# Kernel optimization log

Hardware: AMD Instinct MI355X
Metric: run time of the kernel (lower is better)

Reference implementation:

```python
import jax, jax.numpy as jnp
import numpy as np

N = 10000
E = 160000
IN_CH = 128
HID = 128
HEADS = 4
OUT_CH = 1  # forced by nn.Linear(heads, 1) applied after conv2


def _linear_params(key, out_f, in_f):
    k1, k2 = jax.random.split(key)
    bound = 1.0 / np.sqrt(in_f)
    W = jax.random.uniform(k1, (out_f, in_f), jnp.float32, -bound, bound)
    b = jax.random.uniform(k2, (out_f,), jnp.float32, -bound, bound)
    return W, b


def setup_inputs() -> dict:
    key = jax.random.key(0)
    ks = jax.random.split(key, 12)
    x = jax.random.normal(ks[0], (N, IN_CH), jnp.float32)
    edge_index = jax.random.randint(ks[1], (2, E), 0, N, jnp.int64)

    # conv1: TransformerConv(IN_CH, HID, HEADS)
    Wq1, bq1 = _linear_params(ks[2], HEADS * HID, IN_CH)
    Wk1, bk1 = _linear_params(ks[3], HEADS * HID, IN_CH)
    Wv1, bv1 = _linear_params(ks[4], HEADS * HID, IN_CH)
    Ws1, bs1 = _linear_params(ks[5], HEADS * HID, IN_CH)  # root/skip

    # conv2: TransformerConv(HID*HEADS, OUT_CH, HEADS)
    d2 = HID * HEADS
    Wq2, bq2 = _linear_params(ks[6], HEADS * OUT_CH, d2)
    Wk2, bk2 = _linear_params(ks[7], HEADS * OUT_CH, d2)
    Wv2, bv2 = _linear_params(ks[8], HEADS * OUT_CH, d2)
    Ws2, bs2 = _linear_params(ks[9], HEADS * OUT_CH, d2)

    # final nn.Linear(HEADS, 1)
    Wl, bl = _linear_params(ks[10], 1, HEADS)

    return dict(x=x, edge_index=edge_index,
                Wq1=Wq1, bq1=bq1, Wk1=Wk1, bk1=bk1, Wv1=Wv1, bv1=bv1, Ws1=Ws1, bs1=bs1,
                Wq2=Wq2, bq2=bq2, Wk2=Wk2, bk2=bk2, Wv2=Wv2, bv2=bv2, Ws2=Ws2, bs2=bs2,
                Wl=Wl, bl=bl)


def transformer_conv(x, edge_index, Wq, bq, Wk, bk, Wv, bv, Ws, bs, heads, ch):
    # PyG TransformerConv defaults: concat=True, root_weight=True, beta=False
    n = x.shape[0]
    q = (x @ Wq.T + bq).reshape(n, heads, ch)
    k = (x @ Wk.T + bk).reshape(n, heads, ch)
    v = (x @ Wv.T + bv).reshape(n, heads, ch)

    src, dst = edge_index[0], edge_index[1]  # messages flow src -> dst
    # per-edge attention logits [E, H]
    logits = jnp.einsum('ehc,ehc->eh', q[dst], k[src]) / np.sqrt(ch).astype(np.float32)

    # segment softmax over edges grouped by destination node
    seg_max = jax.ops.segment_max(logits, dst, num_segments=n)  # [N, H]
    seg_max = jnp.where(jnp.isfinite(seg_max), seg_max, 0.0)
    ex = jnp.exp(logits - seg_max[dst])
    denom = jax.ops.segment_sum(ex, dst, num_segments=n)  # [N, H]
    alpha = ex / jnp.maximum(denom[dst], 1e-16)  # [E, H]

    # scatter-aggregate weighted values
    msgs = alpha[:, :, None] * v[src]  # [E, H, C]
    out = jax.ops.segment_sum(msgs, dst, num_segments=n)  # [N, H, C]
    out = out.reshape(n, heads * ch)
    # root/skip connection
    return out + (x @ Ws.T + bs)


def reference(x, edge_index,
              Wq1, bq1, Wk1, bk1, Wv1, bv1, Ws1, bs1,
              Wq2, bq2, Wk2, bk2, Wv2, bv2, Ws2, bs2,
              Wl, bl):
    h = transformer_conv(x, edge_index, Wq1, bq1, Wk1, bk1, Wv1, bv1, Ws1, bs1, HEADS, HID)
    h = jax.nn.relu(h)
    # dropout is identity in eval mode
    h = transformer_conv(h, edge_index, Wq2, bq2, Wk2, bk2, Wv2, bv2, Ws2, bs2, HEADS, OUT_CH)
    h = h @ Wl.T + bl  # [N, 1]
    return jnp.mean(h, axis=0, keepdims=True)  # [1, 1]
```

## Files before the change

### kernel.cpp

```cpp
#include <hip/hip_runtime.h>
#include <math.h>

#define NN 10000
#define NE 160000
#define NROWT 79
#define NCOLT 16
#define NGEMM (NROWT * NCOLT)

typedef __attribute__((ext_vector_type(8))) short bf16x8;
typedef __attribute__((ext_vector_type(4))) float f32x4;
typedef __attribute__((ext_vector_type(2))) float f32x2;

#if defined(__has_builtin)
#if __has_builtin(__builtin_amdgcn_cvt_pk_fp8_f32) && __has_builtin(__builtin_amdgcn_cvt_pk_f32_fp8)
#define HW_FP8 1
#endif
#endif

__device__ inline ushort f2bf(float x) {
  uint u = __float_as_uint(x);
  return (ushort)((u + 0x7fffu + ((u >> 16) & 1u)) >> 16);
}
__device__ inline uint pk2bf(float a, float b) {
  return (uint)f2bf(a) | ((uint)f2bf(b) << 16);
}

__device__ inline void unpack8(uint4 u, float* f) {
  f[0] = __uint_as_float(u.x << 16); f[1] = __uint_as_float(u.x & 0xffff0000u);
  f[2] = __uint_as_float(u.y << 16); f[3] = __uint_as_float(u.y & 0xffff0000u);
  f[4] = __uint_as_float(u.z << 16); f[5] = __uint_as_float(u.z & 0xffff0000u);
  f[6] = __uint_as_float(u.w << 16); f[7] = __uint_as_float(u.w & 0xffff0000u);
}

#ifndef HW_FP8
__device__ inline float fp8_dec1(uint b) {
  uint s = b >> 7, e = (b >> 3) & 15, m = b & 7;
  float v = (e == 0) ? ldexpf((float)m, -9) : ldexpf((float)(8 + m), (int)e - 10);
  return s ? -v : v;
}
__device__ inline uint fp8_enc1(float x) {
  uint s = (__float_as_uint(x) >> 31) << 7;
  float a = fabsf(x);
  if (!(a < 448.f)) return s | 0x7e;
  if (a < 9.765625e-4f) return s;
  int e; float m = frexpf(a, &e);
  int E = e - 1, q;
  if (E < -6) {
    q = (int)rintf(ldexpf(a, 9));
    if (q == 0) return s;
    if (q >= 8) return s | 8;
    return s | (uint)q;
  }
  q = (int)rintf(ldexpf(m, 4));
  if (q == 16) { q = 8; ++E; }
  if (E > 8 || (E == 8 && q == 15)) return s | 0x7e;
  return s | ((uint)(E + 7) << 3) | (uint)(q - 8);
}
#endif

__device__ inline uint pack4_fp8(float a, float b, float c, float d) {
#ifdef HW_FP8
  uint w = (uint)__builtin_amdgcn_cvt_pk_fp8_f32(a, b, 0, false);
  w = (uint)__builtin_amdgcn_cvt_pk_fp8_f32(c, d, (int)w, true);
  return w;
#else
  return fp8_enc1(a) | (fp8_enc1(b) << 8) | (fp8_enc1(c) << 16) | (fp8_enc1(d) << 24);
#endif
}

__device__ inline void dec8_fp8(uint lo, uint hi, float* f) {
#ifdef HW_FP8
  f32x2 p0 = __builtin_amdgcn_cvt_pk_f32_fp8((int)lo, false);
  f32x2 p1 = __builtin_amdgcn_cvt_pk_f32_fp8((int)lo, true);
  f32x2 p2 = __builtin_amdgcn_cvt_pk_f32_fp8((int)hi, false);
  f32x2 p3 = __builtin_amdgcn_cvt_pk_f32_fp8((int)hi, true);
  f[0] = p0.x; f[1] = p0.y; f[2] = p1.x; f[3] = p1.y;
  f[4] = p2.x; f[5] = p2.y; f[6] = p3.x; f[7] = p3.y;
#else
  f[0] = fp8_dec1(lo & 255); f[1] = fp8_dec1((lo >> 8) & 255);
  f[2] = fp8_dec1((lo >> 16) & 255); f[3] = fp8_dec1(lo >> 24);
  f[4] = fp8_dec1(hi & 255); f[5] = fp8_dec1((hi >> 8) & 255);
  f[6] = fp8_dec1((hi >> 16) & 255); f[7] = fp8_dec1(hi >> 24);
#endif
}

__device__ inline void dec16(uint4 u, float* f) {
  dec8_fp8(u.x, u.y, f);
  dec8_fp8(u.z, u.w, f + 8);
}

__global__ __launch_bounds__(1024) void zero_k(
    int* __restrict__ deg, float* __restrict__ out)
{
  int i = blockIdx.x * 1024 + threadIdx.x;
  if (i < NN) deg[i] = 0;
  if (i == 0) out[0] = 0.f;
}

__global__ __launch_bounds__(256) void prep_k(
    const float* __restrict__ x,
    const float* __restrict__ Wq1, const float* __restrict__ Wk1,
    const float* __restrict__ Wv1, const float* __restrict__ Ws1,
    ushort* __restrict__ x_bf, ushort* __restrict__ w1bf,
    const int* __restrict__ dst, int* __restrict__ deg)
{
  int i = blockIdx.x * 256 + threadIdx.x;
  if (i < NE) atomicAdd(&deg[dst[i]], 1);
  const int n4x = NN * 32;
  const int n4w = 512 * 128 / 4;
  if (i < n4x) {
    float4 v = ((const float4*)x)[i];
    ushort4 o;
    o.x = f2bf(v.x); o.y = f2bf(v.y); o.z = f2bf(v.z); o.w = f2bf(v.w);
    ((ushort4*)x_bf)[i] = o;
  } else {
    int c = i - n4x;
    if (c < 4 * n4w) {
      int seg = c >> 14, k = c & 16383;
      const float* W = (seg == 0) ? Wq1 : (seg == 1) ? Wk1
                     : (seg == 2) ? Wv1 : Ws1;
      float4 v = ((const float4*)W)[k];
      ushort4 o;
      o.x = f2bf(v.x); o.y = f2bf(v.y); o.z = f2bf(v.z); o.w = f2bf(v.w);
      ((ushort4*)(w1bf + ((size_t)seg << 16)))[k] = o;
    }
  }
}

__global__ __launch_bounds__(1024) void scan_k(
    const int* __restrict__ deg, int* __restrict__ rowptr,
    int* __restrict__ cursor)
{
  __shared__ int wsum[16];
  int tid = threadIdx.x;
  int base = tid * 10;
  int loc[10]; int s = 0;
  #pragma unroll
  for (int i = 0; i < 10; ++i) {
    int v = (base + i < NN) ? deg[base + i] : 0;
    loc[i] = s; s += v;
  }
  int mysum = s;
  #pragma unroll
  for (int d = 1; d < 64; d <<= 1) {
    int v = __shfl_up(s, d);
    if ((tid & 63) >= d) s += v;
  }
  if ((tid & 63) == 63) wsum[tid >> 6] = s;
  __syncthreads();
  int woff = 0;
  for (int w = 0; w < (tid >> 6); ++w) woff += wsum[w];
  int excl = woff + s - mysum;
  #pragma unroll
  for (int i = 0; i < 10; ++i) {
    int idx = base + i;
    if (idx < NN) { int r = excl + loc[i]; rowptr[idx] = r; cursor[idx] = r; }
  }
  if (tid == 1023) rowptr[NN] = woff + s;
}

__global__ __launch_bounds__(256) void gemm_scatter(
    const ushort* __restrict__ xbf, const ushort* __restrict__ wbf,
    const float* __restrict__ bq, const float* __restrict__ bk,
    const float* __restrict__ bv, const float* __restrict__ bs,
    unsigned char* __restrict__ q8, unsigned char* __restrict__ kv8,
    ushort* __restrict__ h1b,
    const int* __restrict__ src, const int* __restrict__ dst,
    int* __restrict__ cursor, int* __restrict__ csr_src)
{
  if (blockIdx.x >= NGEMM) {
    int e = (blockIdx.x - NGEMM) * 256 + threadIdx.x;
    if (e < NE) {
      int pos = atomicAdd(&cursor[dst[e]], 1);
      csr_src[pos] = src[e];
    }
    return;
  }
  __shared__ __align__(16) ushort LDSbuf[32768];
  ushort* Al = LDSbuf;
  ushort* Bl = LDSbuf + 16384;
  const int row0 = (blockIdx.x % NROWT) << 7;
  const int ncol0 = (blockIdx.x / NROWT) << 7;
  const int tid = threadIdx.x;

  #pragma unroll
  for (int i = 0; i < 8; ++i) {
    int slot = tid + (i << 8);
    int r = slot >> 4, c = slot & 15;
    int gr = row0 + r;
    uint4 v = make_uint4(0u, 0u, 0u, 0u);
    if (gr < NN) v = *(const uint4*)(xbf + (size_t)gr * 128 + (c << 3));
    *(uint4*)(Al + r * 128 + ((c ^ (r & 7)) << 3)) = v;
  }
  #pragma unroll
  for (int i = 0; i < 8; ++i) {
    int slot = tid + (i << 8);
    int r = slot >> 4, c = slot & 15;
    uint4 v = *(const uint4*)(wbf + (size_t)(ncol0 + r) * 128 + (c << 3));
    *(uint4*)(Bl + r * 128 + ((c ^ (r & 7)) << 3)) = v;
  }
  __syncthreads();

  const int wv = tid >> 6, lane = tid & 63;
  const int lr = lane & 15, lkg = lane >> 4;
  const int seg = ncol0 >> 9;
  const int colInSeg = ncol0 & 511;
  const bool swp = (seg < 3);

  f32x4 acc[2][8];
  #pragma unroll
  for (int m = 0; m < 2; ++m)
    #pragma unroll
    for (int n = 0; n < 8; ++n) acc[m][n] = (f32x4){0.f, 0.f, 0.f, 0.f};

  #pragma unroll
  for (int ks = 0; ks < 4; ++ks) {
    int c16 = (ks << 2) + lkg;
    bf16x8 a[2], b[8];
    #pragma unroll
    for (int mf = 0; mf < 2; ++mf) {
      int r = (wv << 5) + (mf << 4) + lr;
      a[mf] = *(const bf16x8*)(Al + r * 128 + ((c16 ^ (r & 7)) << 3));
    }
    #pragma unroll
    for (int nf = 0; nf < 8; ++nf) {
      int r = (nf << 4) + lr;
      b[nf] = *(const bf16x8*)(Bl + r * 128 + ((c16 ^ (r & 7)) << 3));
    }
    if (swp) {
      #pragma unroll
      for (int mf = 0; mf < 2; ++mf)
        #pragma unroll
        for (int nf = 0; nf < 8; ++nf)
          acc[mf][nf] = __builtin_amdgcn_mfma_f32_16x16x32_bf16(
              b[nf], a[mf], acc[mf][nf], 0, 0, 0);
    } else {
      #pragma unroll
      for (int mf = 0; mf < 2; ++mf)
        #pragma unroll
        for (int nf = 0; nf < 8; ++nf)
          acc[mf][nf] = __builtin_amdgcn_mfma_f32_16x16x32_bf16(
              a[mf], b[nf], acc[mf][nf], 0, 0, 0);
    }
  }

  __syncthreads();
  float* S = (float*)LDSbuf;
  const float* bias = (seg == 0) ? bq : (seg == 1) ? bk : (seg == 2) ? bv : bs;

  if (swp) {
    const float scale = (seg == 0) ? 0.08838834764831845f : 1.f;
    unsigned char* out8 = (seg == 0) ? q8 : kv8;
    const int rs = (seg == 0) ? 512 : 1024;
    const int choff = ((seg == 2) ? 512 : 0) + colInSeg;
    #pragma unroll
    for (int pass = 0; pass < 2; ++pass) {
      #pragma unroll
      for (int mf = 0; mf < 2; ++mf) {
        int rl = (wv << 5) + (mf << 4) + lr;
        #pragma unroll
        for (int nf2 = 0; nf2 < 4; ++nf2) {
          int nf = (pass << 2) + nf2;
          int cl = (nf << 4) + (lkg << 2);
          float4 bb = *(const float4*)(bias + colInSeg + cl);
          float4 o;
          o.x = (acc[mf][nf][0] + bb.x) * scale;
          o.y = (acc[mf][nf][1] + bb.y) * scale;
          o.z = (acc[mf][nf][2] + bb.z) * scale;
          o.w = (acc[mf][nf][3] + bb.w) * scale;
          *(float4*)(S + rl * 68 + (cl - (pass << 6))) = o;
        }
      }
      __syncthreads();
      for (int tt = tid; tt < 512; tt += 256) {
        int row = tt >> 2, q4 = (tt & 3) << 4;
        int grow = row0 + row;
        if (grow < NN) {
          const float* p = S + row * 68 + q4;
          uint4 w;
          w.x = pack4_fp8(p[0],  p[1],  p[2],  p[3]);
          w.y = pack4_fp8(p[4],  p[5],  p[6],  p[7]);
          w.z = pack4_fp8(p[8],  p[9],  p[10], p[11]);
          w.w = pack4_fp8(p[12], p[13], p[14], p[15]);
          *(uint4*)(out8 + (size_t)grow * rs + choff + (pass << 6) + q4) = w;
        }
      }
      __syncthreads();
    }
  } else {
    #pragma unroll
    for (int pass = 0; pass < 2; ++pass) {
      #pragma unroll
      for (int mf = 0; mf < 2; ++mf) {
        #pragma unroll
        for (int nf2 = 0; nf2 < 4; ++nf2) {
          int nf = (pass << 2) + nf2;
          int cl = (nf << 4) + lr;
          float bb = bias[colInSeg + cl];
          #pragma unroll
          for (int r = 0; r < 4; ++r) {
            int rl = (wv << 5) + (mf << 4) + (lkg << 2) + r;
            S[rl * 68 + (cl - (pass << 6))] = acc[mf][nf][r] + bb;
          }
        }
      }
      __syncthreads();
      for (int tt = tid; tt < 1024; tt += 256) {
        int row = tt >> 3, g = tt & 7;
        int grow = row0 + row;
        if (grow < NN) {
          const float* p = S + row * 68 + (g << 3);
          uint4 w;
          w.x = pk2bf(p[0], p[1]);
          w.y = pk2bf(p[2], p[3]);
          w.z = pk2bf(p[4], p[5]);
          w.w = pk2bf(p[6], p[7]);
          *(uint4*)(h1b + (size_t)grow * 512 + colInSeg + (pass << 6) + (g << 3)) = w;
        }
      }
      __syncthreads();
    }
  }
}

#define EDGE_A(kvreg)                                                      \
  {                                                                        \
    float f[16]; dec16(kvreg, f);                                          \
    float t = qf[0]*f[0]+qf[1]*f[1]+qf[2]*f[2]+qf[3]*f[3]                  \
            + qf[4]*f[4]+qf[5]*f[5]+qf[6]*f[6]+qf[7]*f[7]                  \
            + qf[8]*f[8]+qf[9]*f[9]+qf[10]*f[10]+qf[11]*f[11]              \
            + qf[12]*f[12]+qf[13]*f[13]+qf[14]*f[14]+qf[15]*f[15];         \
    t += __shfl_xor(t, 1);                                                 \
    t += __shfl_xor(t, 2);                                                 \
    t += __shfl_xor(t, 4);                                                 \
    float exA = __expf(t);                                                 \
    float exO = __shfl_xor(exA, 32);                                       \
    if (kl) den += exA;                                                    \
    float exV = kl ? 0.f : exO;                                            \
    _Pragma("unroll")                                                      \
    for (int i = 0; i < 16; ++i) acc[i] = fmaf(exV, f[i], acc[i]);         \
  }

__global__ __launch_bounds__(256) void attn1(
    const unsigned char* __restrict__ q8, const unsigned char* __restrict__ kv8,
    const int* __restrict__ rowptr, const int* __restrict__ csr_src,
    ushort* __restrict__ h1b)
{
  const int n = blockIdx.x * 4 + (threadIdx.x >> 6);
  const int lane = threadIdx.x & 63;
  const bool kl = lane < 32;
  const int vl = lane & 31;

  float qf[16];
  if (kl) {
    uint4 qv = *(const uint4*)(q8 + (size_t)n * 512 + (lane << 4));
    dec16(qv, qf);
  } else {
    #pragma unroll
    for (int i = 0; i < 16; ++i) qf[i] = 0.f;
  }

  float acc[16] = {};
  float den = 0.f;
  int j = rowptr[n];
  const int e1 = rowptr[n + 1];
  for (; j + 7 < e1; j += 8) {
    uint4 a0 = *(const uint4*)(kv8 + (size_t)csr_src[j + 0] * 1024 + (lane << 4));
    uint4 a1 = *(const uint4*)(kv8 + (size_t)csr_src[j + 1] * 1024 + (lane << 4));
    uint4 a2 = *(const uint4*)(kv8 + (size_t)csr_src[j + 2] * 1024 + (lane << 4));
    uint4 a3 = *(const uint4*)(kv8 + (size_t)csr_src[j + 3] * 1024 + (lane << 4));
    uint4 a4 = *(const uint4*)(kv8 + (size_t)csr_src[j + 4] * 1024 + (lane << 4));
    uint4 a5 = *(const uint4*)(kv8 + (size_t)csr_src[j + 5] * 1024 + (lane << 4));
    uint4 a6 = *(const uint4*)(kv8 + (size_t)csr_src[j + 6] * 1024 + (lane << 4));
    uint4 a7 = *(const uint4*)(kv8 + (size_t)csr_src[j + 7] * 1024 + (lane << 4));
    EDGE_A(a0)
    EDGE_A(a1)
    EDGE_A(a2)
    EDGE_A(a3)
    EDGE_A(a4)
    EDGE_A(a5)
    EDGE_A(a6)
    EDGE_A(a7)
  }
  for (; j + 3 < e1; j += 4) {
    uint4 a0 = *(const uint4*)(kv8 + (size_t)csr_src[j + 0] * 1024 + (lane << 4));
    uint4 a1 = *(const uint4*)(kv8 + (size_t)csr_src[j + 1] * 1024 + (lane << 4));
    uint4 a2 = *(const uint4*)(kv8 + (size_t)csr_src[j + 2] * 1024 + (lane << 4));
    uint4 a3 = *(const uint4*)(kv8 + (size_t)csr_src[j + 3] * 1024 + (lane << 4));
    EDGE_A(a0)
    EDGE_A(a1)
    EDGE_A(a2)
    EDGE_A(a3)
  }
  for (; j < e1; ++j) {
    uint4 a0 = *(const uint4*)(kv8 + (size_t)csr_src[j] * 1024 + (lane << 4));
    EDGE_A(a0)
  }

  float dAll = kl ? den : 0.f;
  float dv = __shfl_xor(dAll, 32);
  if (!kl) {
    float inv = 1.f / fmaxf(dv, 1e-16f);
    int c0 = vl << 4;
    float sk[16];
    uint4 s0 = *(const uint4*)(h1b + (size_t)n * 512 + c0);
    uint4 s1 = *(const uint4*)(h1b + (size_t)n * 512 + c0 + 8);
    unpack8(s0, sk); unpack8(s1, sk + 8);
    ushort o[16];
    #pragma unroll
    for (int i = 0; i < 16; ++i)
      o[i] = f2bf(fmaxf(sk[i] + acc[i] * inv, 0.f));
    uint4 w0, w1;
    w0.x = (uint)o[0]  | ((uint)o[1]  << 16);
    w0.y = (uint)o[2]  | ((uint)o[3]  << 16);
    w0.z = (uint)o[4]  | ((uint)o[5]  << 16);
    w0.w = (uint)o[6]  | ((uint)o[7]  << 16);
    w1.x = (uint)o[8]  | ((uint)o[9]  << 16);
    w1.y = (uint)o[10] | ((uint)o[11] << 16);
    w1.z = (uint)o[12] | ((uint)o[13] << 16);
    w1.w = (uint)o[14] | ((uint)o[15] << 16);
    *(uint4*)(h1b + (size_t)n * 512 + c0) = w0;
    *(uint4*)(h1b + (size_t)n * 512 + c0 + 8) = w1;
  }
}

__global__ __launch_bounds__(256) void gemm_l2(
    const ushort* __restrict__ h1b,
    const float* __restrict__ Wq, const float* __restrict__ bq,
    const float* __restrict__ Wk, const float* __restrict__ bk,
    const float* __restrict__ Wv, const float* __restrict__ bv,
    const float* __restrict__ Ws, const float* __restrict__ bs,
    float* __restrict__ qkv2, float* __restrict__ acc2)
{
  __shared__ float red[4][64][17];
  int n0 = blockIdx.x * 64;
  int wid = threadIdx.x >> 6, lane = threadIdx.x & 63;
  int n = n0 + lane;
  const float* Wm[4] = {Wq, Wk, Wv, Ws};
  float s[16] = {};
  if (n < NN) {
    const ushort* a = h1b + (size_t)n * 512 + wid * 128;
    #pragma unroll 2
    for (int i = 0; i < 128; i += 8) {
      uint4 hv = *(const uint4*)(a + i);
      float av[8]; unpack8(hv, av);
      #pragma unroll
      for (int j = 0; j < 16; ++j) {
        const float* w = Wm[j >> 2] + (size_t)(j & 3) * 512 + wid * 128 + i;
        s[j] += av[0]*w[0] + av[1]*w[1] + av[2]*w[2] + av[3]*w[3]
              + av[4]*w[4] + av[5]*w[5] + av[6]*w[6] + av[7]*w[7];
      }
    }
  }
  #pragma unroll
  for (int j = 0; j < 16; ++j) red[wid][lane][j] = s[j];
  __syncthreads();
  #pragma unroll
  for (int q = 0; q < 4; ++q) {
    int idx = threadIdx.x * 4 + q;
    int ln = idx >> 4, j = idx & 15;
    int nn2 = n0 + ln;
    if (nn2 >= NN) continue;
    float v = red[0][ln][j] + red[1][ln][j] + red[2][ln][j] + red[3][ln][j];
    int sg = j >> 2, r = j & 3;
    const float* bb = (sg == 0) ? bq : (sg == 1) ? bk : (sg == 2) ? bv : bs;
    v += bb[r];
    if (sg < 3) qkv2[nn2 * 12 + sg * 4 + r] = v;
    else        acc2[nn2 * 4 + r] = v;
  }
}

__global__ __launch_bounds__(256) void attn2_final(
    const float* __restrict__ qkv2, const int* __restrict__ rowptr,
    const int* __restrict__ csr_src, const float* __restrict__ acc2,
    const float* __restrict__ Wl, const float* __restrict__ bl,
    float* __restrict__ out)
{
  __shared__ float red[4];
  int t = blockIdx.x * 256 + threadIdx.x;
  int n = t >> 4, h = (t >> 2) & 3, part = t & 3;
  float q = qkv2[n * 12 + h];
  float den = 0.f, acc = 0.f;
  int e1 = rowptr[n + 1];
  for (int j = rowptr[n] + part; j < e1; j += 4) {
    int s = csr_src[j];
    float k = qkv2[s * 12 + 4 + h];
    float v = qkv2[s * 12 + 8 + h];
    float ex = __expf(q * k);
    den += ex; acc += ex * v;
  }
  den += __shfl_xor(den, 1); acc += __shfl_xor(acc, 1);
  den += __shfl_xor(den, 2); acc += __shfl_xor(acc, 2);
  float c = 0.f;
  if (part == 0)
    c = (acc2[n * 4 + h] + acc / fmaxf(den, 1e-16f)) * Wl[h] * (1.0f / NN);
  if (t == 0) c += bl[0];
  c += __shfl_xor(c, 4);
  c += __shfl_xor(c, 8);
  c += __shfl_xor(c, 16);
  c += __shfl_xor(c, 32);
  if ((threadIdx.x & 63) == 0) red[threadIdx.x >> 6] = c;
  __syncthreads();
  if (threadIdx.x == 0)
    unsafeAtomicAdd(out, red[0] + red[1] + red[2] + red[3]);
}

extern "C" void kernel_launch(void* const* d_in, const int* in_sizes, int n_in,
                              void* d_out, int out_size, void* d_ws, size_t ws_size,
                              hipStream_t stream)
{
  const float* x   = (const float*)d_in[0];
  const int*   ei  = (const int*)d_in[1];
  const float *Wq1 = (const float*)d_in[2],  *bq1 = (const float*)d_in[3];
  const float *Wk1 = (const float*)d_in[4],  *bk1 = (const float*)d_in[5];
  const float *Wv1 = (const float*)d_in[6],  *bv1 = (const float*)d_in[7];
  const float *Ws1 = (const float*)d_in[8],  *bs1 = (const float*)d_in[9];
  const float *Wq2 = (const float*)d_in[10], *bq2 = (const float*)d_in[11];
  const float *Wk2 = (const float*)d_in[12], *bk2 = (const float*)d_in[13];
  const float *Wv2 = (const float*)d_in[14], *bv2 = (const float*)d_in[15];
  const float *Ws2 = (const float*)d_in[16], *bs2 = (const float*)d_in[17];
  const float *Wl  = (const float*)d_in[18], *bl  = (const float*)d_in[19];
  const int* srcp = ei;
  const int* dstp = ei + NE;

  unsigned char* q8  = (unsigned char*)d_ws;
  unsigned char* kv8 = q8 + (size_t)NN * 512;
  ushort* x_bf = (ushort*)(kv8 + (size_t)NN * 1024);
  ushort* w1bf = x_bf + (size_t)NN * 128;
  ushort* h1b  = w1bf + (size_t)2048 * 128;
  float*  qkv2 = (float*)(h1b + (size_t)NN * 512);
  float*  acc2 = qkv2 + (size_t)NN * 12;
  int*   deg     = (int*)(acc2 + (size_t)NN * 4);
  int*   rowptr  = deg + NN;
  int*   cursor  = rowptr + NN + 1;
  int*   csr_src = cursor + NN;

  zero_k<<<10, 1024, 0, stream>>>(deg, (float*)d_out);
  {
    const int total = NN * 32 + 4 * (512 * 128 / 4);
    prep_k<<<(total + 255) / 256, 256, 0, stream>>>(
        x, Wq1, Wk1, Wv1, Ws1, x_bf, w1bf, dstp, deg);
  }
  scan_k<<<1, 1024, 0, stream>>>(deg, rowptr, cursor);

  gemm_scatter<<<NGEMM + (NE + 255) / 256, 256, 0, stream>>>(
      x_bf, w1bf, bq1, bk1, bv1, bs1, q8, kv8, h1b,
      srcp, dstp, cursor, csr_src);

  attn1<<<NN / 4, 256, 0, stream>>>(q8, kv8, rowptr, csr_src, h1b);

  gemm_l2<<<(NN + 63) / 64, 256, 0, stream>>>(
      h1b, Wq2, bq2, Wk2, bk2, Wv2, bv2, Ws2, bs2, qkv2, acc2);

  attn2_final<<<NN * 16 / 256, 256, 0, stream>>>(
      qkv2, rowptr, csr_src, acc2, Wl, bl, (float*)d_out);
}
```

Baseline: 131.2 us.

## Fuse layer-1 attention output with layer-2 QKV/skip projection via shared memory

Merges the layer-1 attention kernel and the small layer-2 projection GEMM into one kernel. Each wavefront writes its node's relu'd hidden row (512 floats) into LDS instead of writing bf16 h1b back to global. The block then computes the 16 layer-2 outputs per node directly from LDS, using a 4-way split over K and a shuffle reduction. This removes one kernel launch and the global round trip of the hidden activations. It also keeps the hidden values in fp32 rather than rounding them to bf16. The cost is extra LDS and the weight reads now happen per node inside the attention kernel.

Result: slower. 136.7 us (+4.2%).

```diff
diff --git a/kernel.cpp b/kernel.cpp
--- a/kernel.cpp
+++ b/kernel.cpp
@@ -341,12 +341,19 @@
     for (int i = 0; i < 16; ++i) acc[i] = fmaf(exV, f[i], acc[i]);         \
   }
 
-__global__ __launch_bounds__(256) void attn1(
+__global__ __launch_bounds__(256) void attn_fused(
     const unsigned char* __restrict__ q8, const unsigned char* __restrict__ kv8,
     const int* __restrict__ rowptr, const int* __restrict__ csr_src,
-    ushort* __restrict__ h1b)
-{
-  const int n = blockIdx.x * 4 + (threadIdx.x >> 6);
+    const ushort* __restrict__ h1b,
+    const float* __restrict__ Wq2, const float* __restrict__ bq2,
+    const float* __restrict__ Wk2, const float* __restrict__ bk2,
+    const float* __restrict__ Wv2, const float* __restrict__ bv2,
+    const float* __restrict__ Ws2, const float* __restrict__ bs2,
+    float* __restrict__ qkv2, float* __restrict__ acc2)
+{
+  __shared__ float hl[4][512];
+  const int ns = threadIdx.x >> 6;
+  const int n = blockIdx.x * 4 + ns;
   const int lane = threadIdx.x & 63;
   const bool kl = lane < 32;
   const int vl = lane & 31;
@@ -406,67 +413,33 @@
     uint4 s0 = *(const uint4*)(h1b + (size_t)n * 512 + c0);
     uint4 s1 = *(const uint4*)(h1b + (size_t)n * 512 + c0 + 8);
     unpack8(s0, sk); unpack8(s1, sk + 8);
-    ushort o[16];
     #pragma unroll
     for (int i = 0; i < 16; ++i)
-      o[i] = f2bf(fmaxf(sk[i] + acc[i] * inv, 0.f));
-    uint4 w0, w1;
-    w0.x = (uint)o[0]  | ((uint)o[1]  << 16);
-    w0.y = (uint)o[2]  | ((uint)o[3]  << 16);
-    w0.z = (uint)o[4]  | ((uint)o[5]  << 16);
-    w0.w = (uint)o[6]  | ((uint)o[7]  << 16);
-    w1.x = (uint)o[8]  | ((uint)o[9]  << 16);
-    w1.y = (uint)o[10] | ((uint)o[11] << 16);
-    w1.z = (uint)o[12] | ((uint)o[13] << 16);
-    w1.w = (uint)o[14] | ((uint)o[15] << 16);
-    *(uint4*)(h1b + (size_t)n * 512 + c0) = w0;
-    *(uint4*)(h1b + (size_t)n * 512 + c0 + 8) = w1;
-  }
-}
-
-__global__ __launch_bounds__(256) void gemm_l2(
-    const ushort* __restrict__ h1b,
-    const float* __restrict__ Wq, const float* __restrict__ bq,
-    const float* __restrict__ Wk, const float* __restrict__ bk,
-    const float* __restrict__ Wv, const float* __restrict__ bv,
-    const float* __restrict__ Ws, const float* __restrict__ bs,
-    float* __restrict__ qkv2, float* __restrict__ acc2)
-{
-  __shared__ float red[4][64][17];
-  int n0 = blockIdx.x * 64;
-  int wid = threadIdx.x >> 6, lane = threadIdx.x & 63;
-  int n = n0 + lane;
-  const float* Wm[4] = {Wq, Wk, Wv, Ws};
-  float s[16] = {};
-  if (n < NN) {
-    const ushort* a = h1b + (size_t)n * 512 + wid * 128;
-    #pragma unroll 2
-    for (int i = 0; i < 128; i += 8) {
-      uint4 hv = *(const uint4*)(a + i);
-      float av[8]; unpack8(hv, av);
-      #pragma unroll
-      for (int j = 0; j < 16; ++j) {
-        const float* w = Wm[j >> 2] + (size_t)(j & 3) * 512 + wid * 128 + i;
-        s[j] += av[0]*w[0] + av[1]*w[1] + av[2]*w[2] + av[3]*w[3]
-              + av[4]*w[4] + av[5]*w[5] + av[6]*w[6] + av[7]*w[7];
-      }
-    }
-  }
-  #pragma unroll
-  for (int j = 0; j < 16; ++j) red[wid][lane][j] = s[j];
+      hl[ns][c0 + i] = fmaxf(sk[i] + acc[i] * inv, 0.f);
+  }
   __syncthreads();
-  #pragma unroll
-  for (int q = 0; q < 4; ++q) {
-    int idx = threadIdx.x * 4 + q;
-    int ln = idx >> 4, j = idx & 15;
-    int nn2 = n0 + ln;
-    if (nn2 >= NN) continue;
-    float v = red[0][ln][j] + red[1][ln][j] + red[2][ln][j] + red[3][ln][j];
-    int sg = j >> 2, r = j & 3;
-    const float* bb = (sg == 0) ? bq : (sg == 1) ? bk : (sg == 2) ? bv : bs;
-    v += bb[r];
-    if (sg < 3) qkv2[nn2 * 12 + sg * 4 + r] = v;
-    else        acc2[nn2 * 4 + r] = v;
+
+  {
+    const int j2 = lane & 15, qr = lane >> 4;
+    const float* Wm4[4] = {Wq2, Wk2, Wv2, Ws2};
+    const float* w = Wm4[j2 >> 2] + (size_t)(j2 & 3) * 512 + (qr << 7);
+    const float* h = hl[ns] + (qr << 7);
+    float p = 0.f;
+    #pragma unroll
+    for (int i = 0; i < 128; i += 4) {
+      float4 wv = *(const float4*)(w + i);
+      p += h[i] * wv.x + h[i+1] * wv.y + h[i+2] * wv.z + h[i+3] * wv.w;
+    }
+    p += __shfl_xor(p, 16);
+    p += __shfl_xor(p, 32);
+    if (lane < 16) {
+      int sg = j2 >> 2, r = j2 & 3;
+      const float* bb = (sg == 0) ? bq2 : (sg == 1) ? bk2
+                      : (sg == 2) ? bv2 : bs2;
+      float val = p + bb[r];
+      if (sg < 3) qkv2[n * 12 + sg * 4 + r] = val;
+      else        acc2[n * 4 + r] = val;
+    }
   }
 }
 
@@ -547,10 +520,9 @@
       x_bf, w1bf, bq1, bk1, bv1, bs1, q8, kv8, h1b,
       srcp, dstp, cursor, csr_src);
 
-  attn1<<<NN / 4, 256, 0, stream>>>(q8, kv8, rowptr, csr_src, h1b);
-
-  gemm_l2<<<(NN + 63) / 64, 256, 0, stream>>>(
-      h1b, Wq2, bq2, Wk2, bk2, Wv2, bv2, Ws2, bs2, qkv2, acc2);
+  attn_fused<<<NN / 4, 256, 0, stream>>>(
+      q8, kv8, rowptr, csr_src, h1b,
+      Wq2, bq2, Wk2, bk2, Wv2, bv2, Ws2, bs2, qkv2, acc2);
 
   attn2_final<<<NN * 16 / 256, 256, 0, stream>>>(
       qkv2, rowptr, csr_src, acc2, Wl, bl, (float*)d_out);
```
